# Kernel optimization log

Hardware: AMD Instinct MI355X
Metric: run time of the kernel (lower is better)

Reference implementation:

```python
import jax, jax.numpy as jnp
import numpy as np

SR = 16000
NFFT = 512
NFILT = 64
FRAME_LEN = 400    # 0.025 * 16000
FRAME_STEP = 160   # 0.010 * 16000
NUM_FRAMES = 50000


def _mel_filterbanks():
    # python_speech_features get_filterbanks(nfilt=64, nfft=512, sr=16000, lowfreq=0, highfreq=sr/2)
    def hz2mel(hz):
        return 2595.0 * np.log10(1.0 + hz / 700.0)

    def mel2hz(m):
        return 700.0 * (10.0 ** (m / 2595.0) - 1.0)

    highfreq = SR / 2.0
    melpts = np.linspace(hz2mel(0.0), hz2mel(highfreq), NFILT + 2)
    bins = np.floor((NFFT + 1) * mel2hz(melpts) / SR)
    fb = np.zeros((NFILT, NFFT // 2 + 1), dtype=np.float64)
    for j in range(NFILT):
        for i in range(int(bins[j]), int(bins[j + 1])):
            fb[j, i] = (i - bins[j]) / (bins[j + 1] - bins[j])
        for i in range(int(bins[j + 1]), int(bins[j + 2])):
            fb[j, i] = (bins[j + 2] - i) / (bins[j + 2] - bins[j + 1])
    return fb.T.astype(np.float32)  # (257, nfilt) == filters.T in the original


def setup_inputs() -> dict:
    key = jax.random.key(0)
    audio_len = FRAME_LEN + (NUM_FRAMES - 1) * FRAME_STEP  # 8_000_240 -> exactly 50000 frames, zero pad
    x = jax.random.normal(key, (1, audio_len), dtype=jnp.float32)
    filters = jnp.asarray(_mel_filterbanks())
    return {"x": x, "filters": filters}


def reference(x, filters):
    # pre-emphasis
    x = jnp.concatenate([x[:, :1], x[:, 1:] - 0.97 * x[:, :-1]], axis=1)
    audio_len = x.shape[1]
    num_frames = (audio_len - FRAME_LEN) // FRAME_STEP + 1
    # vectorized framing (replaces the per-frame python slice/stack loop)
    idx = jnp.arange(num_frames)[:, None] * FRAME_STEP + jnp.arange(FRAME_LEN)[None, :]
    windowed = x[:, idx]                                     # (B, F, frame_len)
    r = jnp.fft.rfft(windowed, n=NFFT, axis=2)               # (B, F, nfft//2+1)
    power = (jnp.real(r) ** 2 + jnp.imag(r) ** 2) * (1.0 / NFFT)
    feat = jnp.einsum('bfk,kn->bfn', power, filters) + 1e-30  # (B, F, nfilt)
    # per-frame normalization over (batch, filters), matching reduce_mean/K.std on feat[:, i, :]
    m = jnp.mean(feat, axis=(0, 2), keepdims=True)
    s = jnp.std(feat, axis=(0, 2), keepdims=True)
    feat = (feat - m) / s
    return feat[..., None]                                   # (1, F, nfilt, 1)
```

## Files before the change

### kernel.cpp

```cpp
#include <hip/hip_runtime.h>
#include <math.h>

#define NFILT 64
#define FRAME_LEN 400
#define FRAME_STEP 160
#define WMAX 24
#define WAVES 4
#define NBLOCKS 1024

__global__ __launch_bounds__(256) void fbank_kernel(const float* __restrict__ x,
                                                    const float* __restrict__ filters,
                                                    float* __restrict__ out,
                                                    int num_frames, int fpw) {
    __shared__ float pw[WAVES][280];
    const int t = threadIdx.x;
    const int l = t & 63;
    const int w = t >> 6;
    float* pwrow = pw[w];

    for (int i = 257 + l; i < 280; i += 64) pwrow[i] = 0.0f;

    int lo = 257;
    for (int k = 0; k < 257; k++) {
        float fv = filters[k * NFILT + l];
        if (fv != 0.0f && lo == 257) lo = k;
    }
    if (lo > 256) lo = 256;
    float wc[WMAX];
#pragma unroll
    for (int i = 0; i < WMAX; i++) {
        int k = lo + i;
        wc[i] = (k <= 256) ? filters[k * NFILT + l] : 0.0f;
    }

    const int rl = (int)(__brev((unsigned)l) >> 26);
    float cA[6], sA[6], sg[6];
#pragma unroll
    for (int j = 0; j < 6; j++) {
        const int d = 32 >> j;
        const int hi = l & d;
        float th = -2.0f * (float)M_PI * (float)(l & (d - 1)) / (float)(2 * d);
        cA[j] = hi ? cosf(th) : 1.0f;
        sA[j] = hi ? sinf(th) : 0.0f;
        sg[j] = hi ? -1.0f : 1.0f;
    }
    float br[8], bi[8];
    {
        float th = -2.0f * (float)M_PI * (float)rl * (1.0f / 512.0f);
        float c1 = cosf(th), s1 = sinf(th);
        br[0] = 1.0f; bi[0] = 0.0f; br[1] = c1; bi[1] = s1;
#pragma unroll
        for (int r = 2; r < 8; r++) {
            float pr_ = br[r - 1], pi_ = bi[r - 1];
            br[r] = pr_ * c1 - pi_ * s1;
            bi[r] = pr_ * s1 + pi_ * c1;
        }
    }

    const int gw = blockIdx.x * WAVES + w;
    const long f0 = (long)gw * fpw;
    const long fend = (f0 + fpw < num_frames) ? f0 + fpw : num_frames;

    for (long f = f0; f < fend; f++) {
        const long base = f * FRAME_STEP;

        float a0=0,a1=0,a2=0,a3=0,a4=0,a5=0,a6=0,a7=0;
        if (l < 50) {
            const float4* p4 = reinterpret_cast<const float4*>(x + base + 8 * l);
            float4 A = p4[0], B = p4[1];
            a0=A.x; a1=A.y; a2=A.z; a3=A.w; a4=B.x; a5=B.y; a6=B.z; a7=B.w;
        }
        float prev = __shfl_up(a7, 1, 64);
        if (l == 0) prev = (base > 0) ? x[base - 1] : 0.0f;

        float vr[8], vi[8];
        vr[0] = (l < 50) ? fmaf(-0.97f, prev, a0) : 0.0f;
        vr[1] = (l < 50) ? fmaf(-0.97f, a0, a1) : 0.0f;
        vr[2] = (l < 50) ? fmaf(-0.97f, a1, a2) : 0.0f;
        vr[3] = (l < 50) ? fmaf(-0.97f, a2, a3) : 0.0f;
        vr[4] = (l < 50) ? fmaf(-0.97f, a3, a4) : 0.0f;
        vr[5] = (l < 50) ? fmaf(-0.97f, a4, a5) : 0.0f;
        vr[6] = (l < 50) ? fmaf(-0.97f, a5, a6) : 0.0f;
        vr[7] = (l < 50) ? fmaf(-0.97f, a6, a7) : 0.0f;

#pragma unroll
        for (int r = 0; r < 8; r++) {
            float pr = __shfl_xor(vr[r], 32, 64);
            float tr = fmaf(sg[0], vr[r], pr);
            vr[r] = tr * cA[0];
            vi[r] = tr * sA[0];
        }
#pragma unroll
        for (int j = 1; j < 6; j++) {
            const int d = 32 >> j;
            const float c = cA[j], s = sA[j], g = sg[j];
#pragma unroll
            for (int r = 0; r < 8; r++) {
                float pr = __shfl_xor(vr[r], d, 64);
                float pi = __shfl_xor(vi[r], d, 64);
                float tr = fmaf(g, vr[r], pr);
                float ti = fmaf(g, vi[r], pi);
                vr[r] = tr * c - ti * s;
                vi[r] = tr * s + ti * c;
            }
        }

#pragma unroll
        for (int r = 1; r < 8; r++) {
            float tr = vr[r], ti = vi[r];
            vr[r] = tr * br[r] - ti * bi[r];
            vi[r] = tr * bi[r] + ti * br[r];
        }

        const float RH = 0.70710678118654752f;
        {
            float t0r=vr[0]+vr[4], t0i=vi[0]+vi[4];
            float d0r=vr[0]-vr[4], d0i=vi[0]-vi[4];
            float t1r=vr[1]+vr[5], t1i=vi[1]+vi[5];
            float d1r=vr[1]-vr[5], d1i=vi[1]-vi[5];
            float t2r=vr[2]+vr[6], t2i=vi[2]+vi[6];
            float d2r=vr[2]-vr[6], d2i=vi[2]-vi[6];
            float t3r=vr[3]+vr[7], t3i=vi[3]+vi[7];
            float d3r=vr[3]-vr[7], d3i=vi[3]-vi[7];
            vr[0]=t0r; vi[0]=t0i; vr[1]=t1r; vi[1]=t1i;
            vr[2]=t2r; vi[2]=t2i; vr[3]=t3r; vi[3]=t3i;
            vr[4]=d0r;                 vi[4]=d0i;
            vr[5]=(d1r+d1i)*RH;        vi[5]=(d1i-d1r)*RH;
            vr[6]=d2i;                 vi[6]=-d2r;
            vr[7]=(d3i-d3r)*RH;        vi[7]=-(d3r+d3i)*RH;
        }
        {
            float t0r=vr[0]+vr[2], t0i=vi[0]+vi[2];
            float d0r=vr[0]-vr[2], d0i=vi[0]-vi[2];
            float t1r=vr[1]+vr[3], t1i=vi[1]+vi[3];
            float d1r=vr[1]-vr[3], d1i=vi[1]-vi[3];
            vr[0]=t0r; vi[0]=t0i; vr[1]=t1r; vi[1]=t1i;
            vr[2]=d0r; vi[2]=d0i; vr[3]=d1i; vi[3]=-d1r;
            float t4r=vr[4]+vr[6], t4i=vi[4]+vi[6];
            float d4r=vr[4]-vr[6], d4i=vi[4]-vi[6];
            float t5r=vr[5]+vr[7], t5i=vi[5]+vi[7];
            float d5r=vr[5]-vr[7], d5i=vi[5]-vi[7];
            vr[4]=t4r; vi[4]=t4i; vr[5]=t5r; vi[5]=t5i;
            vr[6]=d4r; vi[6]=d4i; vr[7]=d5i; vi[7]=-d5r;
        }
        {
            float t0r=vr[0]+vr[1], t0i=vi[0]+vi[1];
            float d0r=vr[0]-vr[1], d0i=vi[0]-vi[1];
            vr[0]=t0r; vi[0]=t0i; vr[1]=d0r; vi[1]=d0i;
            float t2r=vr[2]+vr[3], t2i=vi[2]+vi[3];
            float d2r=vr[2]-vr[3], d2i=vi[2]-vi[3];
            vr[2]=t2r; vi[2]=t2i; vr[3]=d2r; vi[3]=d2i;
            float t4r=vr[4]+vr[5], t4i=vi[4]+vi[5];
            float d4r=vr[4]-vr[5], d4i=vi[4]-vi[5];
            vr[4]=t4r; vi[4]=t4i; vr[5]=d4r; vi[5]=d4i;
            float t6r=vr[6]+vr[7], t6i=vi[6]+vi[7];
            float d6r=vr[6]-vr[7], d6i=vi[6]-vi[7];
            vr[6]=t6r; vi[6]=t6i; vr[7]=d6r; vi[7]=d6i;
        }

        const float scale = 1.0f / 512.0f;
        pwrow[rl      ] = (vr[0]*vr[0] + vi[0]*vi[0]) * scale;
        pwrow[rl +  64] = (vr[4]*vr[4] + vi[4]*vi[4]) * scale;
        pwrow[rl + 128] = (vr[2]*vr[2] + vi[2]*vi[2]) * scale;
        pwrow[rl + 192] = (vr[6]*vr[6] + vi[6]*vi[6]) * scale;
        if (l == 0)
            pwrow[256] = (vr[1]*vr[1] + vi[1]*vi[1]) * scale;

        asm volatile("s_waitcnt lgkmcnt(0)" ::: "memory");

        float acc = 1e-30f;
#pragma unroll
        for (int i = 0; i < WMAX; i++)
            acc = fmaf(wc[i], pwrow[lo + i], acc);

        float sum = acc;
#pragma unroll
        for (int mk = 1; mk < 64; mk <<= 1) sum += __shfl_xor(sum, mk, 64);
        const float mean = sum * (1.0f / 64.0f);
        const float dd = acc - mean;
        float v2 = dd * dd;
#pragma unroll
        for (int mk = 1; mk < 64; mk <<= 1) v2 += __shfl_xor(v2, mk, 64);
        const float sd = sqrtf(v2 * (1.0f / 64.0f));
        out[f * NFILT + l] = dd / sd;
    }
}

extern "C" void kernel_launch(void* const* d_in, const int* in_sizes, int n_in,
                              void* d_out, int out_size, void* d_ws, size_t ws_size,
                              hipStream_t stream) {
    (void)d_ws; (void)ws_size; (void)n_in; (void)in_sizes;
    const float* x = (const float*)d_in[0];
    const float* filters = (const float*)d_in[1];
    float* out = (float*)d_out;
    const int num_frames = out_size / NFILT;
    const int total_waves = NBLOCKS * WAVES;
    const int fpw = (num_frames + total_waves - 1) / total_waves;
    fbank_kernel<<<NBLOCKS, 256, 0, stream>>>(x, filters, out, num_frames, fpw);
}
```

Measured before the change: 111.9 us.

## Pack two real frames into one complex FFT and share filter setup via LDS

Each wave now transforms two consecutive frames at once by loading one as the real part and the other as the imaginary part of a single 512-point complex FFT. The two spectra are separated with a conjugate-symmetric shuffle before the mel projection. Filter weights and start indices are computed once per block by wave 0 and kept in LDS instead of being rebuilt by every wave in registers. The launch grows to 1563 blocks with a grid-stride loop over frame pairs. This roughly halves the FFT shuffle and butterfly work per frame, at the cost of extra shuffles for the split, more LDS traffic in the filter dot product, and a block-wide sync.

```diff
diff --git a/kernel.cpp b/kernel.cpp
--- a/kernel.cpp
+++ b/kernel.cpp
@@ -5,32 +5,38 @@
 #define FRAME_LEN 400
 #define FRAME_STEP 160
 #define WMAX 24
+#define WSTRIDE 25
 #define WAVES 4
-#define NBLOCKS 1024
+#define NBLOCKS 1563
+#define PWBINS 280
 
 __global__ __launch_bounds__(256) void fbank_kernel(const float* __restrict__ x,
                                                     const float* __restrict__ filters,
                                                     float* __restrict__ out,
-                                                    int num_frames, int fpw) {
-    __shared__ float pw[WAVES][280];
+                                                    int num_frames) {
+    __shared__ float wc_lds[NFILT * WSTRIDE];
+    __shared__ int   lo_lds[NFILT];
+    __shared__ float pw[WAVES][PWBINS * 2];
+
     const int t = threadIdx.x;
     const int l = t & 63;
     const int w = t >> 6;
     float* pwrow = pw[w];
 
-    for (int i = 257 + l; i < 280; i += 64) pwrow[i] = 0.0f;
-
-    int lo = 257;
-    for (int k = 0; k < 257; k++) {
-        float fv = filters[k * NFILT + l];
-        if (fv != 0.0f && lo == 257) lo = k;
-    }
-    if (lo > 256) lo = 256;
-    float wc[WMAX];
-#pragma unroll
-    for (int i = 0; i < WMAX; i++) {
-        int k = lo + i;
-        wc[i] = (k <= 256) ? filters[k * NFILT + l] : 0.0f;
+    if (l < 2 * (PWBINS - 257)) pwrow[2 * 257 + l] = 0.0f;
+
+    if (w == 0) {
+        int lo = 257;
+        for (int k = 0; k < 257; k++) {
+            float fv = filters[k * NFILT + l];
+            if (fv != 0.0f && lo == 257) lo = k;
+        }
+        if (lo > 256) lo = 256;
+        lo_lds[l] = lo;
+        for (int i = 0; i < WMAX; i++) {
+            int k = lo + i;
+            wc_lds[l * WSTRIDE + i] = (k <= 256) ? filters[k * NFILT + l] : 0.0f;
+        }
     }
 
     const int rl = (int)(__brev((unsigned)l) >> 26);
@@ -56,42 +62,64 @@
             bi[r] = pr_ * s1 + pi_ * c1;
         }
     }
+    const int Lp = (int)(__brev((unsigned)((64 - rl) & 63)) >> 26);
+
+    __syncthreads();
+    const int lo = lo_lds[l];
 
     const int gw = blockIdx.x * WAVES + w;
-    const long f0 = (long)gw * fpw;
-    const long fend = (f0 + fpw < num_frames) ? f0 + fpw : num_frames;
-
-    for (long f = f0; f < fend; f++) {
-        const long base = f * FRAME_STEP;
-
-        float a0=0,a1=0,a2=0,a3=0,a4=0,a5=0,a6=0,a7=0;
-        if (l < 50) {
-            const float4* p4 = reinterpret_cast<const float4*>(x + base + 8 * l);
-            float4 A = p4[0], B = p4[1];
-            a0=A.x; a1=A.y; a2=A.z; a3=A.w; a4=B.x; a5=B.y; a6=B.z; a7=B.w;
-        }
-        float prev = __shfl_up(a7, 1, 64);
-        if (l == 0) prev = (base > 0) ? x[base - 1] : 0.0f;
+    const int totw = gridDim.x * WAVES;
+    const int npairs = (num_frames + 1) >> 1;
+
+    for (int pair = gw; pair < npairs; pair += totw) {
+        const long fa = 2L * pair;
+        const bool hasb = (fa + 1) < num_frames;
+        const long ba = fa * FRAME_STEP;
+        const long bb = ba + FRAME_STEP;
 
         float vr[8], vi[8];
-        vr[0] = (l < 50) ? fmaf(-0.97f, prev, a0) : 0.0f;
-        vr[1] = (l < 50) ? fmaf(-0.97f, a0, a1) : 0.0f;
-        vr[2] = (l < 50) ? fmaf(-0.97f, a1, a2) : 0.0f;
-        vr[3] = (l < 50) ? fmaf(-0.97f, a2, a3) : 0.0f;
-        vr[4] = (l < 50) ? fmaf(-0.97f, a3, a4) : 0.0f;
-        vr[5] = (l < 50) ? fmaf(-0.97f, a4, a5) : 0.0f;
-        vr[6] = (l < 50) ? fmaf(-0.97f, a5, a6) : 0.0f;
-        vr[7] = (l < 50) ? fmaf(-0.97f, a6, a7) : 0.0f;
-
-#pragma unroll
-        for (int r = 0; r < 8; r++) {
-            float pr = __shfl_xor(vr[r], 32, 64);
-            float tr = fmaf(sg[0], vr[r], pr);
-            vr[r] = tr * cA[0];
-            vi[r] = tr * sA[0];
-        }
-#pragma unroll
-        for (int j = 1; j < 6; j++) {
+        {
+            float a0=0,a1=0,a2=0,a3=0,a4=0,a5=0,a6=0,a7=0;
+            if (l < 50) {
+                const float4* p4 = reinterpret_cast<const float4*>(x + ba + 8 * l);
+                float4 A = p4[0], B = p4[1];
+                a0=A.x; a1=A.y; a2=A.z; a3=A.w; a4=B.x; a5=B.y; a6=B.z; a7=B.w;
+            }
+            float ev = x[ba > 0 ? ba - 1 : 0];
+            float edge = (ba > 0) ? ev : 0.0f;
+            float prev = __shfl_up(a7, 1, 64);
+            if (l == 0) prev = edge;
+            vr[0] = (l < 50) ? fmaf(-0.97f, prev, a0) : 0.0f;
+            vr[1] = (l < 50) ? fmaf(-0.97f, a0, a1) : 0.0f;
+            vr[2] = (l < 50) ? fmaf(-0.97f, a1, a2) : 0.0f;
+            vr[3] = (l < 50) ? fmaf(-0.97f, a2, a3) : 0.0f;
+            vr[4] = (l < 50) ? fmaf(-0.97f, a3, a4) : 0.0f;
+            vr[5] = (l < 50) ? fmaf(-0.97f, a4, a5) : 0.0f;
+            vr[6] = (l < 50) ? fmaf(-0.97f, a5, a6) : 0.0f;
+            vr[7] = (l < 50) ? fmaf(-0.97f, a6, a7) : 0.0f;
+        }
+        {
+            float b0=0,b1=0,b2=0,b3=0,b4=0,b5=0,b6=0,b7=0;
+            if (hasb && l < 50) {
+                const float4* p4 = reinterpret_cast<const float4*>(x + bb + 8 * l);
+                float4 A = p4[0], B = p4[1];
+                b0=A.x; b1=A.y; b2=A.z; b3=A.w; b4=B.x; b5=B.y; b6=B.z; b7=B.w;
+            }
+            float edge = hasb ? x[bb - 1] : 0.0f;
+            float prev = __shfl_up(b7, 1, 64);
+            if (l == 0) prev = edge;
+            vi[0] = (l < 50) ? fmaf(-0.97f, prev, b0) : 0.0f;
+            vi[1] = (l < 50) ? fmaf(-0.97f, b0, b1) : 0.0f;
+            vi[2] = (l < 50) ? fmaf(-0.97f, b1, b2) : 0.0f;
+            vi[3] = (l < 50) ? fmaf(-0.97f, b2, b3) : 0.0f;
+            vi[4] = (l < 50) ? fmaf(-0.97f, b3, b4) : 0.0f;
+            vi[5] = (l < 50) ? fmaf(-0.97f, b4, b5) : 0.0f;
+            vi[6] = (l < 50) ? fmaf(-0.97f, b5, b6) : 0.0f;
+            vi[7] = (l < 50) ? fmaf(-0.97f, b6, b7) : 0.0f;
+        }
+
+#pragma unroll
+        for (int j = 0; j < 6; j++) {
             const int d = 32 >> j;
             const float c = cA[j], s = sA[j], g = sg[j];
 #pragma unroll
@@ -158,31 +186,75 @@
             vr[6]=t6r; vi[6]=t6i; vr[7]=d6r; vi[7]=d6i;
         }
 
-        const float scale = 1.0f / 512.0f;
-        pwrow[rl      ] = (vr[0]*vr[0] + vi[0]*vi[0]) * scale;
-        pwrow[rl +  64] = (vr[4]*vr[4] + vi[4]*vi[4]) * scale;
-        pwrow[rl + 128] = (vr[2]*vr[2] + vi[2]*vi[2]) * scale;
-        pwrow[rl + 192] = (vr[6]*vr[6] + vi[6]*vi[6]) * scale;
-        if (l == 0)
-            pwrow[256] = (vr[1]*vr[1] + vi[1]*vi[1]) * scale;
+        float c0r = __shfl(vr[7], Lp, 64), c0i = __shfl(vi[7], Lp, 64);
+        float c1r = __shfl(vr[3], Lp, 64), c1i = __shfl(vi[3], Lp, 64);
+        float c2r = __shfl(vr[5], Lp, 64), c2i = __shfl(vi[5], Lp, 64);
+        float c3r = __shfl(vr[1], Lp, 64), c3i = __shfl(vi[1], Lp, 64);
+        if (l == 0) {
+            c0r = vr[0]; c0i = vi[0];
+            c1r = vr[7]; c1i = vi[7];
+            c2r = vr[3]; c2i = vi[3];
+            c3r = vr[5]; c3i = vi[5];
+        }
+
+        const float S4 = (1.0f / 512.0f) * 0.25f;
+        {
+            float zr = vr[0], zi = vi[0];
+            float e1 = zr + c0r, e2 = zi - c0i, o1 = zi + c0i, o2 = c0r - zr;
+            float2 pq = make_float2((e1*e1 + e2*e2) * S4, (o1*o1 + o2*o2) * S4);
+            *reinterpret_cast<float2*>(&pwrow[2 * rl]) = pq;
+        }
+        {
+            float zr = vr[4], zi = vi[4];
+            float e1 = zr + c1r, e2 = zi - c1i, o1 = zi + c1i, o2 = c1r - zr;
+            float2 pq = make_float2((e1*e1 + e2*e2) * S4, (o1*o1 + o2*o2) * S4);
+            *reinterpret_cast<float2*>(&pwrow[2 * (rl + 64)]) = pq;
+        }
+        {
+            float zr = vr[2], zi = vi[2];
+            float e1 = zr + c2r, e2 = zi - c2i, o1 = zi + c2i, o2 = c2r - zr;
+            float2 pq = make_float2((e1*e1 + e2*e2) * S4, (o1*o1 + o2*o2) * S4);
+            *reinterpret_cast<float2*>(&pwrow[2 * (rl + 128)]) = pq;
+        }
+        {
+            float zr = vr[6], zi = vi[6];
+            float e1 = zr + c3r, e2 = zi - c3i, o1 = zi + c3i, o2 = c3r - zr;
+            float2 pq = make_float2((e1*e1 + e2*e2) * S4, (o1*o1 + o2*o2) * S4);
+            *reinterpret_cast<float2*>(&pwrow[2 * (rl + 192)]) = pq;
+        }
+        if (l == 0) {
+            pwrow[512] = vr[1] * vr[1] * (1.0f / 512.0f);
+            pwrow[513] = vi[1] * vi[1] * (1.0f / 512.0f);
+        }
 
         asm volatile("s_waitcnt lgkmcnt(0)" ::: "memory");
 
-        float acc = 1e-30f;
-#pragma unroll
-        for (int i = 0; i < WMAX; i++)
-            acc = fmaf(wc[i], pwrow[lo + i], acc);
-
-        float sum = acc;
-#pragma unroll
-        for (int mk = 1; mk < 64; mk <<= 1) sum += __shfl_xor(sum, mk, 64);
-        const float mean = sum * (1.0f / 64.0f);
-        const float dd = acc - mean;
-        float v2 = dd * dd;
-#pragma unroll
-        for (int mk = 1; mk < 64; mk <<= 1) v2 += __shfl_xor(v2, mk, 64);
-        const float sd = sqrtf(v2 * (1.0f / 64.0f));
-        out[f * NFILT + l] = dd / sd;
+        float acca = 1e-30f, accb = 1e-30f;
+#pragma unroll
+        for (int i = 0; i < WMAX; i++) {
+            float wv = wc_lds[l * WSTRIDE + i];
+            float2 pq = *reinterpret_cast<const float2*>(&pwrow[2 * (lo + i)]);
+            acca = fmaf(wv, pq.x, acca);
+            accb = fmaf(wv, pq.y, accb);
+        }
+
+        float sa = acca, sb = accb;
+#pragma unroll
+        for (int mk = 1; mk < 64; mk <<= 1) {
+            sa += __shfl_xor(sa, mk, 64);
+            sb += __shfl_xor(sb, mk, 64);
+        }
+        const float ma = sa * (1.0f / 64.0f), mb = sb * (1.0f / 64.0f);
+        const float da = acca - ma, db = accb - mb;
+        float va = da * da, vb = db * db;
+#pragma unroll
+        for (int mk = 1; mk < 64; mk <<= 1) {
+            va += __shfl_xor(va, mk, 64);
+            vb += __shfl_xor(vb, mk, 64);
+        }
+        out[fa * NFILT + l] = da / sqrtf(va * (1.0f / 64.0f));
+        if (hasb)
+            out[(fa + 1) * NFILT + l] = db / sqrtf(vb * (1.0f / 64.0f));
     }
 }
 
@@ -194,7 +266,5 @@
     const float* filters = (const float*)d_in[1];
     float* out = (float*)d_out;
     const int num_frames = out_size / NFILT;
-    const int total_waves = NBLOCKS * WAVES;
-    const int fpw = (num_frames + total_waves - 1) / total_waves;
-    fbank_kernel<<<NBLOCKS, 256, 0, stream>>>(x, filters, out, num_frames, fpw);
+    fbank_kernel<<<NBLOCKS, 256, 0, stream>>>(x, filters, out, num_frames);
 }
```

Result: faster. 102.5 us (-8.4%).
